# Kernel tuning notes

Measured on AMD Instinct MI355X. Metric: run time of the kernel, lower is better.

The kernel has to match this reference:

```python
import jax, jax.numpy as jnp
import numpy as np

INPUT_SIZE = 1024
HIDDEN_SIZE = 2048
BATCH = 4096


def _xavier(key, shape):
    fan_out, fan_in = shape
    std = jnp.sqrt(2.0 / (fan_in + fan_out)).astype(jnp.float32)
    return jax.random.normal(key, shape, dtype=jnp.float32) * std


def setup_inputs() -> dict:
    key = jax.random.key(0)
    ks = jax.random.split(key, 8)
    return {
        "x": jax.random.normal(ks[0], (BATCH, INPUT_SIZE), dtype=jnp.float32),
        "hprev": jax.random.normal(ks[1], (BATCH, HIDDEN_SIZE), dtype=jnp.float32),
        "Wh": _xavier(ks[2], (HIDDEN_SIZE, INPUT_SIZE)),
        "Wz": _xavier(ks[3], (HIDDEN_SIZE, INPUT_SIZE)),
        "Wr": _xavier(ks[4], (HIDDEN_SIZE, INPUT_SIZE)),
        "Uh": _xavier(ks[5], (HIDDEN_SIZE, HIDDEN_SIZE)),
        "Uz": _xavier(ks[6], (HIDDEN_SIZE, HIDDEN_SIZE)),
        "Ur": _xavier(ks[7], (HIDDEN_SIZE, HIDDEN_SIZE)),
        "bh": jnp.zeros((HIDDEN_SIZE,), dtype=jnp.float32),
        "bz": jnp.zeros((HIDDEN_SIZE,), dtype=jnp.float32),
        "br": jnp.zeros((HIDDEN_SIZE,), dtype=jnp.float32),
    }


def reference(x, hprev, Wh, Wz, Wr, Uh, Uz, Ur, bh, bz, br):
    # batched matvec: (b,i) @ (h,i)^T -> (b,h)
    r = jax.nn.sigmoid(x @ Wr.T + hprev @ Ur.T + br)
    z = jax.nn.sigmoid(x @ Wz.T + hprev @ Uz.T + bz)
    h_proposed = jnp.tanh(x @ Wh.T + (r * hprev) @ Uh.T + bh)
    return z * h_proposed + (1.0 - z) * hprev
```

## Files before the change

kernel.cpp:

```cpp
#include <hip/hip_runtime.h>

#define BATCH 4096
#define ISZ   1024
#define HSZ   2048

typedef __bf16 bf16x8 __attribute__((ext_vector_type(8)));
typedef float  f32x4  __attribute__((ext_vector_type(4)));

__device__ __forceinline__ unsigned short f2bf(float f) {
  unsigned u = __builtin_bit_cast(unsigned, f);
  u += 0x7fffu + ((u >> 16) & 1u);
  return (unsigned short)(u >> 16);
}
__device__ __forceinline__ float bf2f(unsigned short s) {
  unsigned u = ((unsigned)s) << 16;
  return __builtin_bit_cast(float, u);
}

struct CvtArgs {
  const float* src[6];
  unsigned short* dst[6];
  int cum[7];
};

__global__ __launch_bounds__(256) void cvt_all_kernel(CvtArgs a, int total4) {
  int i = blockIdx.x * 256 + threadIdx.x;
  if (i >= total4) return;
  int s = 0;
#pragma unroll
  for (int k = 0; k < 5; ++k) s += (i >= a.cum[k + 1]) ? 1 : 0;
  int off = i - a.cum[s];
  float4 f = ((const float4*)a.src[s])[off];
  ushort4 o;
  o.x = f2bf(f.x); o.y = f2bf(f.y); o.z = f2bf(f.z); o.w = f2bf(f.w);
  ((ushort4*)a.dst[s])[off] = o;
}

__device__ __forceinline__ void stage_tile64(const unsigned short* __restrict__ g, int ldK,
                                             int tileRow, int k0, char* lds, int t) {
  char* l0 = lds + ((t >> 6) << 10);
#pragma unroll
  for (int k = 0; k < 4; ++k) {
    int linear = t + k * 256;
    int row = linear >> 3;
    int cs  = linear & 7;
    int c   = cs ^ (row & 7);
    const unsigned short* gp = g + (size_t)(tileRow + row) * ldK + (k0 + c * 8);
    __builtin_amdgcn_global_load_lds((const __attribute__((address_space(1))) void*)gp,
                                     (__attribute__((address_space(3))) void*)(l0 + k * 4096),
                                     16, 0, 0);
  }
}

__device__ __forceinline__ void stage_tile64_w8(const unsigned short* __restrict__ g, int ldK,
                                                int tileRow, int k0, char* lds, int t) {
  char* l0 = lds + ((t >> 6) << 10);
#pragma unroll
  for (int k = 0; k < 2; ++k) {
    int linear = t + k * 512;
    int row = linear >> 3;
    int cs  = linear & 7;
    int c   = cs ^ (row & 7);
    const unsigned short* gp = g + (size_t)(tileRow + row) * ldK + (k0 + c * 8);
    __builtin_amdgcn_global_load_lds((const __attribute__((address_space(1))) void*)gp,
                                     (__attribute__((address_space(3))) void*)(l0 + k * 8192),
                                     16, 0, 0);
  }
}

__device__ __forceinline__ void gemm_seg(const unsigned short* __restrict__ A,
                                         const unsigned short* __restrict__ W,
                                         int K, int rowBase, int colBase,
                                         char* ldsA, char* ldsB,
                                         f32x4 (&acc)[4][4], int t) {
  const int lane = t & 63;
  const int wid  = t >> 6;
  const int wm   = wid >> 1, wn = wid & 1;
  const int lrow = lane & 15;
  const int quad = lane >> 4;
  const int r7   = lrow & 7;
  for (int k0 = 0; k0 < K; k0 += 64) {
    stage_tile64(A, K, rowBase, k0, ldsA, t);
    stage_tile64(W, K, colBase, k0, ldsB, t);
    __syncthreads();
#pragma unroll
    for (int kk = 0; kk < 2; ++kk) {
      const int swz = (((kk << 2) | quad) ^ r7) * 16;
      bf16x8 af[4], bfr[4];
#pragma unroll
      for (int i = 0; i < 4; ++i) {
        af[i]  = *(const bf16x8*)(ldsA + (wm * 64 + i * 16 + lrow) * 128 + swz);
        bfr[i] = *(const bf16x8*)(ldsB + (wn * 64 + i * 16 + lrow) * 128 + swz);
      }
#pragma unroll
      for (int i = 0; i < 4; ++i)
#pragma unroll
        for (int j = 0; j < 4; ++j)
          acc[i][j] = __builtin_amdgcn_mfma_f32_16x16x32_bf16(af[i], bfr[j], acc[i][j], 0, 0, 0);
    }
    __syncthreads();
  }
}

__device__ __forceinline__ void gemm_seg8(const unsigned short* __restrict__ A,
                                          const unsigned short* __restrict__ W,
                                          int K, int rowBase, int colBase,
                                          char* ldsA, char* ldsB,
                                          f32x4 (&acc)[4][2], int t) {
  const int lane = t & 63;
  const int wid  = t >> 6;
  const int wm   = wid >> 2;
  const int wn   = wid & 3;
  const int lrow = lane & 15;
  const int quad = lane >> 4;
  const int r7   = lrow & 7;
  for (int k0 = 0; k0 < K; k0 += 64) {
    stage_tile64_w8(A, K, rowBase, k0, ldsA, t);
    stage_tile64_w8(W, K, colBase, k0, ldsB, t);
    __syncthreads();
#pragma unroll
    for (int kk = 0; kk < 2; ++kk) {
      const int swz = (((kk << 2) | quad) ^ r7) * 16;
      bf16x8 af[4], bfr[2];
#pragma unroll
      for (int i = 0; i < 4; ++i)
        af[i]  = *(const bf16x8*)(ldsA + (wm * 64 + i * 16 + lrow) * 128 + swz);
#pragma unroll
      for (int j = 0; j < 2; ++j)
        bfr[j] = *(const bf16x8*)(ldsB + (wn * 32 + j * 16 + lrow) * 128 + swz);
#pragma unroll
      for (int i = 0; i < 4; ++i)
#pragma unroll
        for (int j = 0; j < 2; ++j)
          acc[i][j] = __builtin_amdgcn_mfma_f32_16x16x32_bf16(af[i], bfr[j], acc[i][j], 0, 0, 0);
    }
    __syncthreads();
  }
}

__device__ __forceinline__ float fast_sigmoid(float v) {
  return 1.0f / (1.0f + __expf(-v));
}
__device__ __forceinline__ float fast_tanh(float v) {
  float e = __expf(2.0f * v);
  return 1.0f - 2.0f / (e + 1.0f);
}

__global__ __launch_bounds__(256, 4) void gate_rz(
    const unsigned short* __restrict__ xb, const unsigned short* __restrict__ hb,
    const unsigned short* __restrict__ Wr, const unsigned short* __restrict__ Ur,
    const unsigned short* __restrict__ Wz, const unsigned short* __restrict__ Uz,
    const float* __restrict__ br, const float* __restrict__ bz,
    const float* __restrict__ Wh32, const float* __restrict__ Uh32,
    unsigned short* __restrict__ Whb, unsigned short* __restrict__ Uhb,
    unsigned short* __restrict__ rh, unsigned short* __restrict__ Zbuf) {
  __shared__ char lds[32768];
  const int t = threadIdx.x;

  if (blockIdx.z == 0) {
    const int NW = (HSZ * ISZ) / 4;
    const int NU = (HSZ * HSZ) / 4;
    int tid = (blockIdx.x + (blockIdx.y << 4)) * 256 + t;
    for (int i = tid; i < NW + NU; i += 512 * 256) {
      const float4* s4 = (i < NW) ? (const float4*)Wh32 + i
                                  : (const float4*)Uh32 + (i - NW);
      ushort4* d4 = (i < NW) ? (ushort4*)Whb + i
                             : (ushort4*)Uhb + (i - NW);
      float4 f = *s4;
      ushort4 o;
      o.x = f2bf(f.x); o.y = f2bf(f.y); o.z = f2bf(f.z); o.w = f2bf(f.w);
      *d4 = o;
    }
    return;
  }

  char* ldsA = lds;
  char* ldsB = lds + 16384;
  int lin = blockIdx.x + (blockIdx.y << 4) + ((blockIdx.z - 1) << 9);
  int xcd = lin & 7, s = lin >> 3;
  int bx = xcd * 2 + (s & 1);
  int by = (s >> 1) & 31;
  int bz_ = s >> 6;

  const int rowBase = by * 128;
  const int colBase = bx * 128;
  const bool isZ = (bz_ != 0);
  const unsigned short* W = isZ ? Wz : Wr;
  const unsigned short* U = isZ ? Uz : Ur;
  const float* biasP = isZ ? bz : br;

  f32x4 acc[4][4];
#pragma unroll
  for (int i = 0; i < 4; ++i)
#pragma unroll
    for (int j = 0; j < 4; ++j)
      acc[i][j] = (f32x4){0.f, 0.f, 0.f, 0.f};

  gemm_seg(xb, W, ISZ, rowBase, colBase, ldsA, ldsB, acc, t);
  gemm_seg(hb, U, HSZ, rowBase, colBase, ldsA, ldsB, acc, t);

  const int lane = t & 63, wid = t >> 6;
  const int wm = wid >> 1, wn = wid & 1, lrow = lane & 15, quad = lane >> 4;
#pragma unroll
  for (int i = 0; i < 4; ++i) {
#pragma unroll
    for (int j = 0; j < 4; ++j) {
      int col = colBase + wn * 64 + j * 16 + lrow;
      float bv = biasP[col];
#pragma unroll
      for (int r = 0; r < 4; ++r) {
        int row = rowBase + wm * 64 + i * 16 + quad * 4 + r;
        float sg = fast_sigmoid(acc[i][j][r] + bv);
        int idx = row * HSZ + col;
        if (isZ) {
          Zbuf[idx] = f2bf(sg);
        } else {
          rh[idx] = f2bf(sg * bf2f(hb[idx]));
        }
      }
    }
  }
}

__global__ __launch_bounds__(512, 4) void gate_h(
    const unsigned short* __restrict__ xb, const unsigned short* __restrict__ rhb,
    const unsigned short* __restrict__ Wh, const unsigned short* __restrict__ Uh,
    const float* __restrict__ bh, const unsigned short* __restrict__ Zbuf,
    const float* __restrict__ hprev, float* __restrict__ out) {
  __shared__ char lds[32768];
  char* ldsA = lds;
  char* ldsB = lds + 16384;
  const int t = threadIdx.x;

  int lin = blockIdx.x + (blockIdx.y << 4);
  int xcd = lin & 7, s = lin >> 3;
  int bx = xcd * 2 + (s & 1);
  int by = s >> 1;

  const int rowBase = by * 128;
  const int colBase = bx * 128;

  f32x4 acc[4][2];
#pragma unroll
  for (int i = 0; i < 4; ++i)
#pragma unroll
    for (int j = 0; j < 2; ++j)
      acc[i][j] = (f32x4){0.f, 0.f, 0.f, 0.f};

  gemm_seg8(xb, Wh, ISZ, rowBase, colBase, ldsA, ldsB, acc, t);
  gemm_seg8(rhb, Uh, HSZ, rowBase, colBase, ldsA, ldsB, acc, t);

  const int lane = t & 63, wid = t >> 6;
  const int wm = wid >> 2, wn = wid & 3, lrow = lane & 15, quad = lane >> 4;
#pragma unroll
  for (int i = 0; i < 4; ++i) {
#pragma unroll
    for (int j = 0; j < 2; ++j) {
      int col = colBase + wn * 32 + j * 16 + lrow;
      float bv = bh[col];
#pragma unroll
      for (int r = 0; r < 4; ++r) {
        int row = rowBase + wm * 64 + i * 16 + quad * 4 + r;
        float hp = fast_tanh(acc[i][j][r] + bv);
        int idx = row * HSZ + col;
        float z = bf2f(Zbuf[idx]);
        float h = hprev[idx];
        out[idx] = h + z * (hp - h);
      }
    }
  }
}

extern "C" void kernel_launch(void* const* d_in, const int* in_sizes, int n_in,
                              void* d_out, int out_size, void* d_ws, size_t ws_size,
                              hipStream_t stream) {
  (void)in_sizes; (void)n_in; (void)out_size; (void)ws_size;
  const float* x     = (const float*)d_in[0];
  const float* hprev = (const float*)d_in[1];
  const float* Wh    = (const float*)d_in[2];
  const float* Wz    = (const float*)d_in[3];
  const float* Wr    = (const float*)d_in[4];
  const float* Uh    = (const float*)d_in[5];
  const float* Uz    = (const float*)d_in[6];
  const float* Ur    = (const float*)d_in[7];
  const float* bh    = (const float*)d_in[8];
  const float* bz    = (const float*)d_in[9];
  const float* br    = (const float*)d_in[10];
  float* out = (float*)d_out;

  char* ws = (char*)d_ws;
  size_t off = 0;
  auto alloc = [&](size_t bytes) { char* p = ws + off; off += bytes; return p; };
  unsigned short* xb  = (unsigned short*)alloc((size_t)BATCH * ISZ * 2);
  unsigned short* hb  = (unsigned short*)alloc((size_t)BATCH * HSZ * 2);
  unsigned short* Wrb = (unsigned short*)alloc((size_t)HSZ * ISZ * 2);
  unsigned short* Wzb = (unsigned short*)alloc((size_t)HSZ * ISZ * 2);
  unsigned short* Whb = (unsigned short*)alloc((size_t)HSZ * ISZ * 2);
  unsigned short* Urb = (unsigned short*)alloc((size_t)HSZ * HSZ * 2);
  unsigned short* Uzb = (unsigned short*)alloc((size_t)HSZ * HSZ * 2);
  unsigned short* Uhb = (unsigned short*)alloc((size_t)HSZ * HSZ * 2);
  unsigned short* rhb = (unsigned short*)alloc((size_t)BATCH * HSZ * 2);
  unsigned short* Zb  = (unsigned short*)alloc((size_t)BATCH * HSZ * 2);

  CvtArgs ca;
  const float* srcs[6]      = {x, hprev, Wr, Wz, Ur, Uz};
  unsigned short* dsts[6]   = {xb, hb, Wrb, Wzb, Urb, Uzb};
  int n4s[6] = {BATCH * ISZ / 4, BATCH * HSZ / 4,
                HSZ * ISZ / 4, HSZ * ISZ / 4,
                HSZ * HSZ / 4, HSZ * HSZ / 4};
  int cum = 0;
  for (int i = 0; i < 6; ++i) {
    ca.src[i] = srcs[i];
    ca.dst[i] = dsts[i];
    ca.cum[i] = cum;
    cum += n4s[i];
  }
  ca.cum[6] = cum;
  cvt_all_kernel<<<(cum + 255) / 256, 256, 0, stream>>>(ca, cum);

  dim3 gridA(HSZ / 128, BATCH / 128, 3);
  gate_rz<<<gridA, 256, 0, stream>>>(xb, hb, Wrb, Urb, Wzb, Uzb, br, bz,
                                     Wh, Uh, Whb, Uhb, rhb, Zb);

  dim3 gridB(HSZ / 128, BATCH / 128, 1);
  gate_h<<<gridB, 512, 0, stream>>>(xb, rhb, Whb, Uhb, bh, Zb, hprev, out);
}
```

Measured before the change: 342.7 us.

## Rewrite gate GEMMs with larger tiles and double-buffered async LDS pipeline

Replaces the single-buffered 128x128 GEMM loops with 256x256 (rz) and 128x256 (h) block tiles using 512 threads. Global-to-LDS loads are issued into double buffers interleaved with MFMA phases, using explicit vmcnt waits, barriers and setprio. The Wh/Uh weight conversion moves out of gate_rz into the shared conversion kernel. Larger tiles cut global traffic per FLOP and the prefetch hides load latency. In exchange the grids drop to 256 blocks each and the kernels use much more LDS and registers, which can hurt occupancy and wave-count balance across the CUs.

```diff
diff --git a/kernel.cpp b/kernel.cpp
--- a/kernel.cpp
+++ b/kernel.cpp
@@ -17,10 +17,15 @@
   return __builtin_bit_cast(float, u);
 }
 
+__device__ __forceinline__ void gll16(const unsigned short* gp, char* lp) {
+  __builtin_amdgcn_global_load_lds((const __attribute__((address_space(1))) void*)gp,
+                                   (__attribute__((address_space(3))) void*)lp, 16, 0, 0);
+}
+
 struct CvtArgs {
-  const float* src[6];
-  unsigned short* dst[6];
-  int cum[7];
+  const float* src[8];
+  unsigned short* dst[8];
+  int cum[9];
 };
 
 __global__ __launch_bounds__(256) void cvt_all_kernel(CvtArgs a, int total4) {
@@ -28,7 +33,7 @@
   if (i >= total4) return;
   int s = 0;
 #pragma unroll
-  for (int k = 0; k < 5; ++k) s += (i >= a.cum[k + 1]) ? 1 : 0;
+  for (int k = 0; k < 7; ++k) s += (i >= a.cum[k + 1]) ? 1 : 0;
   int off = i - a.cum[s];
   float4 f = ((const float4*)a.src[s])[off];
   ushort4 o;
@@ -36,232 +41,266 @@
   ((ushort4*)a.dst[s])[off] = o;
 }
 
-__device__ __forceinline__ void stage_tile64(const unsigned short* __restrict__ g, int ldK,
-                                             int tileRow, int k0, char* lds, int t) {
-  char* l0 = lds + ((t >> 6) << 10);
-#pragma unroll
-  for (int k = 0; k < 4; ++k) {
-    int linear = t + k * 256;
-    int row = linear >> 3;
-    int cs  = linear & 7;
-    int c   = cs ^ (row & 7);
-    const unsigned short* gp = g + (size_t)(tileRow + row) * ldK + (k0 + c * 8);
-    __builtin_amdgcn_global_load_lds((const __attribute__((address_space(1))) void*)gp,
-                                     (__attribute__((address_space(3))) void*)(l0 + k * 4096),
-                                     16, 0, 0);
-  }
-}
-
-__device__ __forceinline__ void stage_tile64_w8(const unsigned short* __restrict__ g, int ldK,
-                                                int tileRow, int k0, char* lds, int t) {
-  char* l0 = lds + ((t >> 6) << 10);
-#pragma unroll
-  for (int k = 0; k < 2; ++k) {
-    int linear = t + k * 512;
-    int row = linear >> 3;
-    int cs  = linear & 7;
-    int c   = cs ^ (row & 7);
-    const unsigned short* gp = g + (size_t)(tileRow + row) * ldK + (k0 + c * 8);
-    __builtin_amdgcn_global_load_lds((const __attribute__((address_space(1))) void*)gp,
-                                     (__attribute__((address_space(3))) void*)(l0 + k * 8192),
-                                     16, 0, 0);
-  }
-}
-
-__device__ __forceinline__ void gemm_seg(const unsigned short* __restrict__ A,
-                                         const unsigned short* __restrict__ W,
-                                         int K, int rowBase, int colBase,
-                                         char* ldsA, char* ldsB,
-                                         f32x4 (&acc)[4][4], int t) {
-  const int lane = t & 63;
-  const int wid  = t >> 6;
-  const int wm   = wid >> 1, wn = wid & 1;
-  const int lrow = lane & 15;
-  const int quad = lane >> 4;
-  const int r7   = lrow & 7;
-  for (int k0 = 0; k0 < K; k0 += 64) {
-    stage_tile64(A, K, rowBase, k0, ldsA, t);
-    stage_tile64(W, K, colBase, k0, ldsB, t);
-    __syncthreads();
-#pragma unroll
-    for (int kk = 0; kk < 2; ++kk) {
-      const int swz = (((kk << 2) | quad) ^ r7) * 16;
-      bf16x8 af[4], bfr[4];
-#pragma unroll
-      for (int i = 0; i < 4; ++i) {
-        af[i]  = *(const bf16x8*)(ldsA + (wm * 64 + i * 16 + lrow) * 128 + swz);
-        bfr[i] = *(const bf16x8*)(ldsB + (wn * 64 + i * 16 + lrow) * 128 + swz);
-      }
-#pragma unroll
-      for (int i = 0; i < 4; ++i)
-#pragma unroll
-        for (int j = 0; j < 4; ++j)
-          acc[i][j] = __builtin_amdgcn_mfma_f32_16x16x32_bf16(af[i], bfr[j], acc[i][j], 0, 0, 0);
-    }
-    __syncthreads();
-  }
-}
-
-__device__ __forceinline__ void gemm_seg8(const unsigned short* __restrict__ A,
-                                          const unsigned short* __restrict__ W,
-                                          int K, int rowBase, int colBase,
-                                          char* ldsA, char* ldsB,
-                                          f32x4 (&acc)[4][2], int t) {
-  const int lane = t & 63;
-  const int wid  = t >> 6;
-  const int wm   = wid >> 2;
-  const int wn   = wid & 3;
-  const int lrow = lane & 15;
-  const int quad = lane >> 4;
-  const int r7   = lrow & 7;
-  for (int k0 = 0; k0 < K; k0 += 64) {
-    stage_tile64_w8(A, K, rowBase, k0, ldsA, t);
-    stage_tile64_w8(W, K, colBase, k0, ldsB, t);
-    __syncthreads();
-#pragma unroll
-    for (int kk = 0; kk < 2; ++kk) {
-      const int swz = (((kk << 2) | quad) ^ r7) * 16;
-      bf16x8 af[4], bfr[2];
-#pragma unroll
-      for (int i = 0; i < 4; ++i)
-        af[i]  = *(const bf16x8*)(ldsA + (wm * 64 + i * 16 + lrow) * 128 + swz);
-#pragma unroll
-      for (int j = 0; j < 2; ++j)
-        bfr[j] = *(const bf16x8*)(ldsB + (wn * 32 + j * 16 + lrow) * 128 + swz);
-#pragma unroll
-      for (int i = 0; i < 4; ++i)
-#pragma unroll
-        for (int j = 0; j < 2; ++j)
-          acc[i][j] = __builtin_amdgcn_mfma_f32_16x16x32_bf16(af[i], bfr[j], acc[i][j], 0, 0, 0);
-    }
-    __syncthreads();
-  }
-}
-
-__device__ __forceinline__ float fast_sigmoid(float v) {
-  return 1.0f / (1.0f + __expf(-v));
-}
-__device__ __forceinline__ float fast_tanh(float v) {
-  float e = __expf(2.0f * v);
-  return 1.0f - 2.0f / (e + 1.0f);
-}
-
-__global__ __launch_bounds__(256, 4) void gate_rz(
+
+__device__ __forceinline__ void stageS64(const unsigned short* __restrict__ g, int ldK,
+                                         int base, int k0, char* tile, int h, int t) {
+  int r = t >> 3;
+  int c = (t & 7) ^ (r & 7);
+  const unsigned short* gp = g + (size_t)(base + h * 64 + r) * ldK + (k0 + c * 8);
+  char* l0 = tile + (h * 64 + ((t >> 6) << 3)) * 128;
+  gll16(gp, l0);
+  gll16(gp + (size_t)128 * ldK, l0 + 16384);
+}
+
+template <int NLOAD>
+__device__ __forceinline__ void stageS32(const unsigned short* __restrict__ g, int ldK,
+                                         int base, int k0, char* tile, int h, int t) {
+#pragma unroll
+  for (int k = 0; k < NLOAD; ++k) {
+    int r = (t >> 3) + k * 64;
+    int c = (t & 7) ^ (r & 7);
+    int row = h * 32 + (r & 31) + ((r >> 5) << 6);
+    const unsigned short* gp = g + (size_t)(base + row) * ldK + (k0 + c * 8);
+    int rw = ((t >> 6) << 3) + k * 64;
+    char* l0 = tile + (h * 32 + (rw & 31) + ((rw >> 5) << 6)) * 128;
+    gll16(gp, l0);
+  }
+}
+
+#define BAR() __builtin_amdgcn_s_barrier()
+#define VMW4() asm volatile("s_waitcnt vmcnt(4)" ::: "memory")
+#define VMW3() asm volatile("s_waitcnt vmcnt(3)" ::: "memory")
+
+#define LDA_RZ(bA, IH)                                                               \
+  _Pragma("unroll") for (int kk = 0; kk < 2; ++kk) {                                 \
+    const int swz = (((kk << 2) | quad) ^ r7) << 4;                                  \
+    _Pragma("unroll") for (int ii = 0; ii < 4; ++ii)                                 \
+      aF[ii][kk] = *(const bf16x8*)((bA) + (wm * 128 + (IH) * 64 + ii * 16 + lrow) * 128 + swz); \
+  }
+#define LDB_RZ(bB, JH, BF)                                                           \
+  _Pragma("unroll") for (int kk = 0; kk < 2; ++kk) {                                 \
+    const int swz = (((kk << 2) | quad) ^ r7) << 4;                                  \
+    _Pragma("unroll") for (int jj = 0; jj < 2; ++jj)                                 \
+      BF[jj][kk] = *(const bf16x8*)((bB) + (wn * 64 + (JH) * 32 + jj * 16 + lrow) * 128 + swz); \
+  }
+#define MMA_RZ(IH, JH, BF)                                                           \
+  __builtin_amdgcn_s_setprio(1);                                                     \
+  _Pragma("unroll") for (int kk = 0; kk < 2; ++kk)                                   \
+    _Pragma("unroll") for (int ii = 0; ii < 4; ++ii)                                 \
+      _Pragma("unroll") for (int jj = 0; jj < 2; ++jj)                               \
+        acc[(IH) * 4 + ii][(JH) * 2 + jj] = __builtin_amdgcn_mfma_f32_16x16x32_bf16( \
+            aF[ii][kk], BF[jj][kk], acc[(IH) * 4 + ii][(JH) * 2 + jj], 0, 0, 0);     \
+  __builtin_amdgcn_s_setprio(0);
+
+__global__ __launch_bounds__(512, 2) void gate_rz(
     const unsigned short* __restrict__ xb, const unsigned short* __restrict__ hb,
     const unsigned short* __restrict__ Wr, const unsigned short* __restrict__ Ur,
     const unsigned short* __restrict__ Wz, const unsigned short* __restrict__ Uz,
     const float* __restrict__ br, const float* __restrict__ bz,
-    const float* __restrict__ Wh32, const float* __restrict__ Uh32,
-    unsigned short* __restrict__ Whb, unsigned short* __restrict__ Uhb,
     unsigned short* __restrict__ rh, unsigned short* __restrict__ Zbuf) {
-  __shared__ char lds[32768];
+  extern __shared__ char lds[];
+  char* A0 = lds;
+  char* B0 = lds + 32768;
+  char* A1 = lds + 65536;
+  char* B1 = lds + 98304;
+
   const int t = threadIdx.x;
-
-  if (blockIdx.z == 0) {
-    const int NW = (HSZ * ISZ) / 4;
-    const int NU = (HSZ * HSZ) / 4;
-    int tid = (blockIdx.x + (blockIdx.y << 4)) * 256 + t;
-    for (int i = tid; i < NW + NU; i += 512 * 256) {
-      const float4* s4 = (i < NW) ? (const float4*)Wh32 + i
-                                  : (const float4*)Uh32 + (i - NW);
-      ushort4* d4 = (i < NW) ? (ushort4*)Whb + i
-                             : (ushort4*)Uhb + (i - NW);
-      float4 f = *s4;
-      ushort4 o;
-      o.x = f2bf(f.x); o.y = f2bf(f.y); o.z = f2bf(f.z); o.w = f2bf(f.w);
-      *d4 = o;
-    }
-    return;
-  }
-
-  char* ldsA = lds;
-  char* ldsB = lds + 16384;
-  int lin = blockIdx.x + (blockIdx.y << 4) + ((blockIdx.z - 1) << 9);
-  int xcd = lin & 7, s = lin >> 3;
-  int bx = xcd * 2 + (s & 1);
-  int by = (s >> 1) & 31;
-  int bz_ = s >> 6;
-
-  const int rowBase = by * 128;
-  const int colBase = bx * 128;
-  const bool isZ = (bz_ != 0);
-  const unsigned short* W = isZ ? Wz : Wr;
-  const unsigned short* U = isZ ? Uz : Ur;
-  const float* biasP = isZ ? bz : br;
-
-  f32x4 acc[4][4];
-#pragma unroll
-  for (int i = 0; i < 4; ++i)
+  const int lane = t & 63, wid = t >> 6;
+  const int wm = wid >> 2, wn = wid & 3;
+  const int lrow = lane & 15, quad = lane >> 4, r7 = lrow & 7;
+
+  int lin = blockIdx.x + (blockIdx.y << 3);
+  int x = lin & 7, s = lin >> 3;
+  const int gate = x >> 2;
+  const int colBase = ((((x & 3) << 1) | (s & 1))) * 256;
+  const int rowBase = (s >> 1) * 256;
+  const unsigned short* W = gate ? Wz : Wr;
+  const unsigned short* U = gate ? Uz : Ur;
+  const float* bias = gate ? bz : br;
+
+  const int NT = (ISZ + HSZ) / 64;
+
+  auto prefA = [&](int tt, char* dst, int h) {
+    tt = tt < NT ? tt : NT - 1;
+    if (tt < ISZ / 64) stageS64(xb, ISZ, rowBase, tt * 64, dst, h, t);
+    else               stageS64(hb, HSZ, rowBase, (tt - ISZ / 64) * 64, dst, h, t);
+  };
+  auto prefB = [&](int tt, char* dst, int h) {
+    tt = tt < NT ? tt : NT - 1;
+    if (tt < ISZ / 64) stageS32<2>(W, ISZ, colBase, tt * 64, dst, h, t);
+    else               stageS32<2>(U, HSZ, colBase, (tt - ISZ / 64) * 64, dst, h, t);
+  };
+
+  f32x4 acc[8][4];
+#pragma unroll
+  for (int i = 0; i < 8; ++i)
 #pragma unroll
     for (int j = 0; j < 4; ++j)
       acc[i][j] = (f32x4){0.f, 0.f, 0.f, 0.f};
 
-  gemm_seg(xb, W, ISZ, rowBase, colBase, ldsA, ldsB, acc, t);
-  gemm_seg(hb, U, HSZ, rowBase, colBase, ldsA, ldsB, acc, t);
-
-  const int lane = t & 63, wid = t >> 6;
-  const int wm = wid >> 1, wn = wid & 1, lrow = lane & 15, quad = lane >> 4;
-#pragma unroll
-  for (int i = 0; i < 4; ++i) {
+  prefA(0, A0, 0); prefB(0, B0, 0);
+  prefA(0, A0, 1); prefB(0, B0, 1);
+  prefA(1, A1, 0); prefB(1, B1, 0);
+  VMW4();
+  BAR();
+
+#pragma unroll 1
+  for (int it = 0; it < NT / 2; ++it) {
+    const int t0 = 2 * it, t1 = 2 * it + 1;
+    bf16x8 aF[4][2], bF0[2][2], bF1[2][2];
+    LDA_RZ(A0, 0); LDB_RZ(B0, 0, bF0);
+    prefA(t1, A1, 1);
+    BAR(); MMA_RZ(0, 0, bF0); BAR();
+    LDB_RZ(B0, 1, bF1);
+    prefB(t1, B1, 1);
+    BAR(); MMA_RZ(0, 1, bF1); BAR();
+    LDA_RZ(A0, 1);
+    prefA(t0 + 2, A0, 0);
+    BAR(); MMA_RZ(1, 0, bF0); BAR();
+    prefB(t0 + 2, B0, 0);
+    VMW4();
+    BAR(); MMA_RZ(1, 1, bF1); BAR();
+    LDA_RZ(A1, 0); LDB_RZ(B1, 0, bF0);
+    prefA(t0 + 2, A0, 1);
+    BAR(); MMA_RZ(0, 0, bF0); BAR();
+    LDB_RZ(B1, 1, bF1);
+    prefB(t0 + 2, B0, 1);
+    BAR(); MMA_RZ(0, 1, bF1); BAR();
+    LDA_RZ(A1, 1);
+    prefA(t1 + 2, A1, 0);
+    BAR(); MMA_RZ(1, 0, bF0); BAR();
+    prefB(t1 + 2, B1, 0);
+    VMW4();
+    BAR(); MMA_RZ(1, 1, bF1); BAR();
+  }
+
+#pragma unroll
+  for (int i = 0; i < 8; ++i) {
 #pragma unroll
     for (int j = 0; j < 4; ++j) {
       int col = colBase + wn * 64 + j * 16 + lrow;
-      float bv = biasP[col];
+      float bv = bias[col];
 #pragma unroll
       for (int r = 0; r < 4; ++r) {
-        int row = rowBase + wm * 64 + i * 16 + quad * 4 + r;
-        float sg = fast_sigmoid(acc[i][j][r] + bv);
+        int row = rowBase + wm * 128 + i * 16 + quad * 4 + r;
+        float sg = 1.0f / (1.0f + __expf(-(acc[i][j][r] + bv)));
         int idx = row * HSZ + col;
-        if (isZ) {
-          Zbuf[idx] = f2bf(sg);
-        } else {
-          rh[idx] = f2bf(sg * bf2f(hb[idx]));
-        }
+        if (gate) Zbuf[idx] = f2bf(sg);
+        else      rh[idx]   = f2bf(sg * bf2f(hb[idx]));
       }
     }
   }
 }
 
-__global__ __launch_bounds__(512, 4) void gate_h(
+#define LDA_H(bA, IH)                                                                \
+  _Pragma("unroll") for (int kk = 0; kk < 2; ++kk) {                                 \
+    const int swz = (((kk << 2) | quad) ^ r7) << 4;                                  \
+    _Pragma("unroll") for (int ii = 0; ii < 2; ++ii)                                 \
+      aF[ii][kk] = *(const bf16x8*)((bA) + (wm * 64 + (IH) * 32 + ii * 16 + lrow) * 128 + swz); \
+  }
+#define LDB_H(bB, JH, BF)                                                            \
+  _Pragma("unroll") for (int kk = 0; kk < 2; ++kk) {                                 \
+    const int swz = (((kk << 2) | quad) ^ r7) << 4;                                  \
+    _Pragma("unroll") for (int jj = 0; jj < 2; ++jj)                                 \
+      BF[jj][kk] = *(const bf16x8*)((bB) + (wn * 64 + (JH) * 32 + jj * 16 + lrow) * 128 + swz); \
+  }
+#define MMA_H(IH, JH, BF)                                                            \
+  __builtin_amdgcn_s_setprio(1);                                                     \
+  _Pragma("unroll") for (int kk = 0; kk < 2; ++kk)                                   \
+    _Pragma("unroll") for (int ii = 0; ii < 2; ++ii)                                 \
+      _Pragma("unroll") for (int jj = 0; jj < 2; ++jj)                               \
+        acc[(IH) * 2 + ii][(JH) * 2 + jj] = __builtin_amdgcn_mfma_f32_16x16x32_bf16( \
+            aF[ii][kk], BF[jj][kk], acc[(IH) * 2 + ii][(JH) * 2 + jj], 0, 0, 0);     \
+  __builtin_amdgcn_s_setprio(0);
+
+__global__ __launch_bounds__(512, 2) void gate_h(
     const unsigned short* __restrict__ xb, const unsigned short* __restrict__ rhb,
     const unsigned short* __restrict__ Wh, const unsigned short* __restrict__ Uh,
     const float* __restrict__ bh, const unsigned short* __restrict__ Zbuf,
     const float* __restrict__ hprev, float* __restrict__ out) {
-  __shared__ char lds[32768];
-  char* ldsA = lds;
-  char* ldsB = lds + 16384;
+  extern __shared__ char lds[];
+  char* A0 = lds;
+  char* A1 = lds + 16384;
+  char* B0 = lds + 32768;
+  char* B1 = lds + 65536;
+
   const int t = threadIdx.x;
-
-  int lin = blockIdx.x + (blockIdx.y << 4);
-  int xcd = lin & 7, s = lin >> 3;
-  int bx = xcd * 2 + (s & 1);
-  int by = s >> 1;
-
-  const int rowBase = by * 128;
-  const int colBase = bx * 128;
-
-  f32x4 acc[4][2];
+  const int lane = t & 63, wid = t >> 6;
+  const int wm = wid >> 2, wn = wid & 3;
+  const int lrow = lane & 15, quad = lane >> 4, r7 = lrow & 7;
+
+  int lin = blockIdx.x + (blockIdx.y << 3);
+  const int colBase = (lin & 7) * 256;
+  const int rowBase = (lin >> 3) * 128;
+
+  const int NT = (ISZ + HSZ) / 64;
+
+  auto prefA = [&](int tt, char* dst, int h) {
+    tt = tt < NT ? tt : NT - 1;
+    if (tt < ISZ / 64) stageS32<1>(xb,  ISZ, rowBase, tt * 64, dst, h, t);
+    else               stageS32<1>(rhb, HSZ, rowBase, (tt - ISZ / 64) * 64, dst, h, t);
+  };
+  auto prefB = [&](int tt, char* dst, int h) {
+    tt = tt < NT ? tt : NT - 1;
+    if (tt < ISZ / 64) stageS32<2>(Wh, ISZ, colBase, tt * 64, dst, h, t);
+    else               stageS32<2>(Uh, HSZ, colBase, (tt - ISZ / 64) * 64, dst, h, t);
+  };
+
+  f32x4 acc[4][4];
 #pragma unroll
   for (int i = 0; i < 4; ++i)
 #pragma unroll
-    for (int j = 0; j < 2; ++j)
+    for (int j = 0; j < 4; ++j)
       acc[i][j] = (f32x4){0.f, 0.f, 0.f, 0.f};
 
-  gemm_seg8(xb, Wh, ISZ, rowBase, colBase, ldsA, ldsB, acc, t);
-  gemm_seg8(rhb, Uh, HSZ, rowBase, colBase, ldsA, ldsB, acc, t);
-
-  const int lane = t & 63, wid = t >> 6;
-  const int wm = wid >> 2, wn = wid & 3, lrow = lane & 15, quad = lane >> 4;
+  prefA(0, A0, 0); prefB(0, B0, 0);
+  prefA(0, A0, 1); prefB(0, B0, 1);
+  prefA(1, A1, 0); prefB(1, B1, 0);
+  VMW3();
+  BAR();
+
+#pragma unroll 1
+  for (int it = 0; it < NT / 2; ++it) {
+    const int t0 = 2 * it, t1 = 2 * it + 1;
+    bf16x8 aF[2][2], bF0[2][2], bF1[2][2];
+    LDA_H(A0, 0); LDB_H(B0, 0, bF0);
+    prefA(t1, A1, 1);
+    BAR(); MMA_H(0, 0, bF0); BAR();
+    LDB_H(B0, 1, bF1);
+    prefB(t1, B1, 1);
+    BAR(); MMA_H(0, 1, bF1); BAR();
+    LDA_H(A0, 1);
+    prefA(t0 + 2, A0, 0);
+    BAR(); MMA_H(1, 0, bF0); BAR();
+    prefB(t0 + 2, B0, 0);
+    VMW3();
+    BAR(); MMA_H(1, 1, bF1); BAR();
+    LDA_H(A1, 0); LDB_H(B1, 0, bF0);
+    prefA(t0 + 2, A0, 1);
+    BAR(); MMA_H(0, 0, bF0); BAR();
+    LDB_H(B1, 1, bF1);
+    prefB(t0 + 2, B0, 1);
+    BAR(); MMA_H(0, 1, bF1); BAR();
+    LDA_H(A1, 1);
+    prefA(t1 + 2, A1, 0);
+    BAR(); MMA_H(1, 0, bF0); BAR();
+    prefB(t1 + 2, B1, 0);
+    VMW3();
+    BAR(); MMA_H(1, 1, bF1); BAR();
+  }
+
 #pragma unroll
   for (int i = 0; i < 4; ++i) {
 #pragma unroll
-    for (int j = 0; j < 2; ++j) {
-      int col = colBase + wn * 32 + j * 16 + lrow;
+    for (int j = 0; j < 4; ++j) {
+      int col = colBase + wn * 64 + j * 16 + lrow;
       float bv = bh[col];
 #pragma unroll
       for (int r = 0; r < 4; ++r) {
         int row = rowBase + wm * 64 + i * 16 + quad * 4 + r;
-        float hp = fast_tanh(acc[i][j][r] + bv);
+        float v = acc[i][j][r] + bv;
+        float e = __expf(2.0f * v);
+        float hp = 1.0f - 2.0f / (e + 1.0f);
         int idx = row * HSZ + col;
         float z = bf2f(Zbuf[idx]);
         float h = hprev[idx];
@@ -302,26 +341,33 @@
   unsigned short* rhb = (unsigned short*)alloc((size_t)BATCH * HSZ * 2);
   unsigned short* Zb  = (unsigned short*)alloc((size_t)BATCH * HSZ * 2);
 
+  static int attrs_done = 0;
+  if (!attrs_done) {
+    hipFuncSetAttribute((const void*)gate_rz, hipFuncAttributeMaxDynamicSharedMemorySize, 131072);
+    hipFuncSetAttribute((const void*)gate_h,  hipFuncAttributeMaxDynamicSharedMemorySize, 98304);
+    attrs_done = 1;
+  }
+
   CvtArgs ca;
-  const float* srcs[6]      = {x, hprev, Wr, Wz, Ur, Uz};
-  unsigned short* dsts[6]   = {xb, hb, Wrb, Wzb, Urb, Uzb};
-  int n4s[6] = {BATCH * ISZ / 4, BATCH * HSZ / 4,
+  const float* srcs[8]    = {x, hprev, Wr, Wz, Ur, Uz, Wh, Uh};
+  unsigned short* dsts[8] = {xb, hb, Wrb, Wzb, Urb, Uzb, Whb, Uhb};
+  int n4s[8] = {BATCH * ISZ / 4, BATCH * HSZ / 4,
                 HSZ * ISZ / 4, HSZ * ISZ / 4,
-                HSZ * HSZ / 4, HSZ * HSZ / 4};
+                HSZ * HSZ / 4, HSZ * HSZ / 4,
+                HSZ * ISZ / 4, HSZ * HSZ / 4};
   int cum = 0;
-  for (int i = 0; i < 6; ++i) {
+  for (int i = 0; i < 8; ++i) {
     ca.src[i] = srcs[i];
     ca.dst[i] = dsts[i];
     ca.cum[i] = cum;
     cum += n4s[i];
   }
-  ca.cum[6] = cum;
+  ca.cum[8] = cum;
   cvt_all_kernel<<<(cum + 255) / 256, 256, 0, stream>>>(ca, cum);
 
-  dim3 gridA(HSZ / 128, BATCH / 128, 3);
-  gate_rz<<<gridA, 256, 0, stream>>>(xb, hb, Wrb, Urb, Wzb, Uzb, br, bz,
-                                     Wh, Uh, Whb, Uhb, rhb, Zb);
-
-  dim3 gridB(HSZ / 128, BATCH / 128, 1);
-  gate_h<<<gridB, 512, 0, stream>>>(xb, rhb, Whb, Uhb, bh, Zb, hprev, out);
-}
+  dim3 gridA(8, 32, 1);
+  gate_rz<<<gridA, 512, 131072, stream>>>(xb, hb, Wrb, Urb, Wzb, Uzb, br, bz, rhb, Zb);
+
+  dim3 gridB(8, 32, 1);
+  gate_h<<<gridB, 512, 98304, stream>>>(xb, rhb, Whb, Uhb, bh, Zb, hprev, out);
+}
```

Result: slower. 354.8 us (+3.5%).

## Fuse r and z gate GEMMs to share A tiles in one block

Applied to the files above, without the earlier changes.

Each gate_rz block now computes both the r and z gate tiles for the same 128x128 output region. It stages the shared x/hprev A tile once per k-step and keeps two accumulator sets. This halves the block count and the repeated A-tile loads. In exchange it doubles accumulator registers and raises LDS to 48KB per block, with the launch bound occupancy hint lowered from 4 to 2.

```diff
diff --git a/kernel.cpp b/kernel.cpp
--- a/kernel.cpp
+++ b/kernel.cpp
@@ -68,11 +68,12 @@
   }
 }
 
-__device__ __forceinline__ void gemm_seg(const unsigned short* __restrict__ A,
-                                         const unsigned short* __restrict__ W,
-                                         int K, int rowBase, int colBase,
-                                         char* ldsA, char* ldsB,
-                                         f32x4 (&acc)[4][4], int t) {
+__device__ __forceinline__ void gemm_seg_rz(const unsigned short* __restrict__ A,
+                                            const unsigned short* __restrict__ Br,
+                                            const unsigned short* __restrict__ Bz,
+                                            int K, int rowBase, int colBase,
+                                            char* ldsA, char* ldsBr, char* ldsBz,
+                                            f32x4 (&accR)[4][4], f32x4 (&accZ)[4][4], int t) {
   const int lane = t & 63;
   const int wid  = t >> 6;
   const int wm   = wid >> 1, wn = wid & 1;
@@ -80,23 +81,33 @@
   const int quad = lane >> 4;
   const int r7   = lrow & 7;
   for (int k0 = 0; k0 < K; k0 += 64) {
-    stage_tile64(A, K, rowBase, k0, ldsA, t);
-    stage_tile64(W, K, colBase, k0, ldsB, t);
+    stage_tile64(A,  K, rowBase, k0, ldsA,  t);
+    stage_tile64(Br, K, colBase, k0, ldsBr, t);
+    stage_tile64(Bz, K, colBase, k0, ldsBz, t);
     __syncthreads();
 #pragma unroll
     for (int kk = 0; kk < 2; ++kk) {
       const int swz = (((kk << 2) | quad) ^ r7) * 16;
       bf16x8 af[4], bfr[4];
 #pragma unroll
-      for (int i = 0; i < 4; ++i) {
-        af[i]  = *(const bf16x8*)(ldsA + (wm * 64 + i * 16 + lrow) * 128 + swz);
-        bfr[i] = *(const bf16x8*)(ldsB + (wn * 64 + i * 16 + lrow) * 128 + swz);
-      }
+      for (int i = 0; i < 4; ++i)
+        af[i] = *(const bf16x8*)(ldsA + (wm * 64 + i * 16 + lrow) * 128 + swz);
+#pragma unroll
+      for (int j = 0; j < 4; ++j)
+        bfr[j] = *(const bf16x8*)(ldsBr + (wn * 64 + j * 16 + lrow) * 128 + swz);
 #pragma unroll
       for (int i = 0; i < 4; ++i)
 #pragma unroll
         for (int j = 0; j < 4; ++j)
-          acc[i][j] = __builtin_amdgcn_mfma_f32_16x16x32_bf16(af[i], bfr[j], acc[i][j], 0, 0, 0);
+          accR[i][j] = __builtin_amdgcn_mfma_f32_16x16x32_bf16(af[i], bfr[j], accR[i][j], 0, 0, 0);
+#pragma unroll
+      for (int j = 0; j < 4; ++j)
+        bfr[j] = *(const bf16x8*)(ldsBz + (wn * 64 + j * 16 + lrow) * 128 + swz);
+#pragma unroll
+      for (int i = 0; i < 4; ++i)
+#pragma unroll
+        for (int j = 0; j < 4; ++j)
+          accZ[i][j] = __builtin_amdgcn_mfma_f32_16x16x32_bf16(af[i], bfr[j], accZ[i][j], 0, 0, 0);
     }
     __syncthreads();
   }
@@ -146,7 +157,7 @@
   return 1.0f - 2.0f / (e + 1.0f);
 }
 
-__global__ __launch_bounds__(256, 4) void gate_rz(
+__global__ __launch_bounds__(256, 2) void gate_rz(
     const unsigned short* __restrict__ xb, const unsigned short* __restrict__ hb,
     const unsigned short* __restrict__ Wr, const unsigned short* __restrict__ Ur,
     const unsigned short* __restrict__ Wz, const unsigned short* __restrict__ Uz,
@@ -154,7 +165,7 @@
     const float* __restrict__ Wh32, const float* __restrict__ Uh32,
     unsigned short* __restrict__ Whb, unsigned short* __restrict__ Uhb,
     unsigned short* __restrict__ rh, unsigned short* __restrict__ Zbuf) {
-  __shared__ char lds[32768];
+  __shared__ char lds[49152];
   const int t = threadIdx.x;
 
   if (blockIdx.z == 0) {
@@ -174,30 +185,29 @@
     return;
   }
 
-  char* ldsA = lds;
-  char* ldsB = lds + 16384;
-  int lin = blockIdx.x + (blockIdx.y << 4) + ((blockIdx.z - 1) << 9);
+  char* ldsA  = lds;
+  char* ldsBr = lds + 16384;
+  char* ldsBz = lds + 32768;
+
+  int lin = blockIdx.x + (blockIdx.y << 4);
   int xcd = lin & 7, s = lin >> 3;
   int bx = xcd * 2 + (s & 1);
-  int by = (s >> 1) & 31;
-  int bz_ = s >> 6;
+  int by = s >> 1;
 
   const int rowBase = by * 128;
   const int colBase = bx * 128;
-  const bool isZ = (bz_ != 0);
-  const unsigned short* W = isZ ? Wz : Wr;
-  const unsigned short* U = isZ ? Uz : Ur;
-  const float* biasP = isZ ? bz : br;
-
-  f32x4 acc[4][4];
+
+  f32x4 accR[4][4], accZ[4][4];
 #pragma unroll
   for (int i = 0; i < 4; ++i)
 #pragma unroll
-    for (int j = 0; j < 4; ++j)
-      acc[i][j] = (f32x4){0.f, 0.f, 0.f, 0.f};
-
-  gemm_seg(xb, W, ISZ, rowBase, colBase, ldsA, ldsB, acc, t);
-  gemm_seg(hb, U, HSZ, rowBase, colBase, ldsA, ldsB, acc, t);
+    for (int j = 0; j < 4; ++j) {
+      accR[i][j] = (f32x4){0.f, 0.f, 0.f, 0.f};
+      accZ[i][j] = (f32x4){0.f, 0.f, 0.f, 0.f};
+    }
+
+  gemm_seg_rz(xb, Wr, Wz, ISZ, rowBase, colBase, ldsA, ldsBr, ldsBz, accR, accZ, t);
+  gemm_seg_rz(hb, Ur, Uz, HSZ, rowBase, colBase, ldsA, ldsBr, ldsBz, accR, accZ, t);
 
   const int lane = t & 63, wid = t >> 6;
   const int wm = wid >> 1, wn = wid & 1, lrow = lane & 15, quad = lane >> 4;
@@ -206,17 +216,17 @@
 #pragma unroll
     for (int j = 0; j < 4; ++j) {
       int col = colBase + wn * 64 + j * 16 + lrow;
-      float bv = biasP[col];
+      float bvr = br[col];
+      float bvz = bz[col];
 #pragma unroll
       for (int r = 0; r < 4; ++r) {
         int row = rowBase + wm * 64 + i * 16 + quad * 4 + r;
-        float sg = fast_sigmoid(acc[i][j][r] + bv);
         int idx = row * HSZ + col;
-        if (isZ) {
-          Zbuf[idx] = f2bf(sg);
-        } else {
-          rh[idx] = f2bf(sg * bf2f(hb[idx]));
-        }
+        float hv = bf2f(hb[idx]);
+        float sr = fast_sigmoid(accR[i][j][r] + bvr);
+        float sz = fast_sigmoid(accZ[i][j][r] + bvz);
+        rh[idx]   = f2bf(sr * hv);
+        Zbuf[idx] = f2bf(sz);
       }
     }
   }
@@ -318,7 +328,7 @@
   ca.cum[6] = cum;
   cvt_all_kernel<<<(cum + 255) / 256, 256, 0, stream>>>(ca, cum);
 
-  dim3 gridA(HSZ / 128, BATCH / 128, 3);
+  dim3 gridA(HSZ / 128, BATCH / 128, 2);
   gate_rz<<<gridA, 256, 0, stream>>>(xb, hb, Wrb, Urb, Wzb, Uzb, br, bz,
                                      Wh, Uh, Whb, Uhb, rhb, Zb);
 
```

Result: faster. 328.9 us (-4.0%).
